# Optimization experiments

Hardware: AMD Instinct MI355X
Metric: run time of the kernel (lower is better)

Reference implementation:

```python
import jax, jax.numpy as jnp
import numpy as np

# config matching init_kwargs
WS = 7          # window side -> N = 49 tokens
NUM_HEADS = 8
DIM = 256
N = WS * WS     # 49
NW = 64         # windows per image (56x56 feature map / 7x7 windows)
B = 64          # images
B_ = B * NW     # 4096 window-batches


def _relative_position_index():
    # exact replica of the numpy construction in __init__
    coords_h = np.arange(WS)
    coords_w = np.arange(WS)
    coords = np.stack(np.meshgrid(coords_h, coords_w, indexing='ij'))  # (2, WS, WS)
    coords_flatten = coords.reshape(2, -1)                             # (2, N)
    rel = coords_flatten[:, :, None] - coords_flatten[:, None, :]      # (2, N, N)
    rel = rel.transpose(1, 2, 0)                                       # (N, N, 2)
    rel[:, :, 0] += WS - 1
    rel[:, :, 1] += WS - 1
    rel[:, :, 0] *= 2 * WS - 1
    return rel.sum(-1).astype(np.int32)                                # (N, N) in [0, 169)


def setup_inputs() -> dict:
    key = jax.random.key(0)
    k1, k2, k3 = jax.random.split(key, 3)
    x = jax.random.normal(k1, (B_, N, DIM), dtype=jnp.float32)
    bias_table = jax.random.normal(k2, (169, NUM_HEADS), dtype=jnp.float32) * 0.02
    mask = jax.random.normal(k3, (NW, N, N), dtype=jnp.float32)
    rel_index = jnp.asarray(_relative_position_index())
    return {"x": x, "bias_table": bias_table, "mask": mask, "rel_index": rel_index}


def reference(x, bias_table, mask, rel_index):
    B_, n, C = x.shape
    head_dim = C // NUM_HEADS
    scale = head_dim ** -0.5
    # NOTE: original call() uses x_qkv[0] for q, k AND v (qkv Dense never applied)
    qkv = x.reshape(B_, n, NUM_HEADS, head_dim).transpose(0, 2, 1, 3)  # (B_, H, N, hd)
    attn = jnp.einsum('bhid,bhjd->bhij', qkv * scale, qkv)             # (B_, H, N, N)
    # gathered relative-position bias: (N*N, H) -> (H, N, N)
    bias = bias_table[rel_index.reshape(-1)].reshape(n, n, NUM_HEADS).transpose(2, 0, 1)
    attn = attn + bias[None]
    # additive window mask: (nW, N, N) broadcast over batch and heads
    nW = mask.shape[0]
    attn = attn.reshape(B_ // nW, nW, NUM_HEADS, n, n) + mask[None, :, None]
    attn = jax.nn.softmax(attn.reshape(B_, NUM_HEADS, n, n), axis=-1)
    out = jnp.einsum('bhij,bhjd->bhid', attn, qkv)                     # (B_, H, N, hd)
    return out.transpose(0, 2, 1, 3).reshape(B_, n, C)
```

## Files before the change

kernel.cpp:

```cpp
#include <hip/hip_runtime.h>
#include <hip/hip_bf16.h>

typedef float f32x4 __attribute__((ext_vector_type(4)));
typedef short s16x8 __attribute__((ext_vector_type(8)));

#define LOG2E 1.4426950408889634f
#define NEGINF (-1e30f)

__device__ __forceinline__ unsigned short f2bf(float f) {
    __hip_bfloat16 h = __float2bfloat16(f);
    unsigned short u;
    __builtin_memcpy(&u, &h, 2);
    return u;
}

__global__ void fuse_bias_mask(const float* __restrict__ bias_table,
                               const float* __restrict__ mask,
                               const int*   __restrict__ rel_index,
                               float*       __restrict__ fused) {
    int tid = blockIdx.x * 256 + threadIdx.x;
    const int total = 512 * 2401;
    if (tid >= total) return;
    int wh  = tid / 2401;
    int rem = tid - wh * 2401;
    int c   = rem / 49;
    int w = wh >> 3, h = wh & 7;
    int idx = rel_index[rem];
    float v = (mask[w * 2401 + rem] + bias_table[idx * 8 + h]) * LOG2E;
    fused[((long)wh * 49 + c) * 52 + (rem - c * 49)] = v;
}

template<bool FUSED>
__global__ __launch_bounds__(256, 2)
void win_attn(const float* __restrict__ x,
              const float* __restrict__ bias_table,
              const float* __restrict__ mask,
              const int*   __restrict__ rel_index,
              const float* __restrict__ fused,
              float*       __restrict__ out) {
    __shared__ char Plds[4][8192];
    const int tid  = threadIdx.x;
    const int wav  = tid >> 6;
    const int lane = tid & 63;
    const int li   = lane & 15;
    const int g    = lane >> 4;
    const int b    = blockIdx.x;
    const int w    = b & 63;
    char* P = &Plds[wav][0];
    const float scale2 = 0.17677669529663689f * LOG2E;

    const float* xb = x + (long)b * (49 * 256);

    for (int hh = 0; hh < 2; ++hh) {
        const int h = wav * 2 + hh;
        const float* xh = xb + h * 32;

        s16x8 Fh[4], Fl[4];
        #pragma unroll
        for (int t = 0; t < 4; ++t) {
            int row = t * 16 + li;
            float f[8];
            if (row < 49) {
                const f32x4* p = (const f32x4*)(xh + row * 256 + g * 8);
                f32x4 v0 = p[0], v1 = p[1];
                f[0]=v0.x; f[1]=v0.y; f[2]=v0.z; f[3]=v0.w;
                f[4]=v1.x; f[5]=v1.y; f[6]=v1.z; f[7]=v1.w;
            } else {
                #pragma unroll
                for (int j = 0; j < 8; ++j) f[j] = 0.f;
            }
            s16x8 hi, lo;
            #pragma unroll
            for (int j = 0; j < 8; ++j) {
                unsigned u = __float_as_uint(f[j]);
                hi[j] = (short)(u >> 16);
                float rm = f[j] - __uint_as_float(u & 0xFFFF0000u);
                lo[j] = (short)f2bf(rm);
            }
            Fh[t] = hi; Fl[t] = lo;
        }

        s16x8 Vf[2][2];
        #pragma unroll
        for (int nd = 0; nd < 2; ++nd)
            #pragma unroll
            for (int kt = 0; kt < 2; ++kt) {
                int d = li + 16 * nd;
                s16x8 vv;
                #pragma unroll
                for (int jj = 0; jj < 8; ++jj) {
                    int j = 32 * kt + 8 * g + jj;
                    float v = (j < 49) ? xh[j * 256 + d] : 0.f;
                    vv[jj] = (short)f2bf(v);
                }
                Vf[nd][kt] = vv;
            }

        f32x4 acc[4][4];
        #pragma unroll
        for (int mr = 0; mr < 4; ++mr)
            #pragma unroll
            for (int nc = 0; nc < 4; ++nc)
                acc[mr][nc] = f32x4{0.f, 0.f, 0.f, 0.f};
        #pragma unroll
        for (int mr = 0; mr < 4; ++mr)
            #pragma unroll
            for (int nc = 0; nc < 4; ++nc) {
                f32x4 a = acc[mr][nc];
                a = __builtin_amdgcn_mfma_f32_16x16x32_bf16(Fh[mr], Fh[nc], a, 0, 0, 0);
                a = __builtin_amdgcn_mfma_f32_16x16x32_bf16(Fh[mr], Fl[nc], a, 0, 0, 0);
                a = __builtin_amdgcn_mfma_f32_16x16x32_bf16(Fl[mr], Fh[nc], a, 0, 0, 0);
                acc[mr][nc] = a;
            }

        const int wh = w * 8 + h;
        #pragma unroll
        for (int nc = 0; nc < 4; ++nc) {
            int c = li + 16 * nc;
            int cidx = min(c, 48);
            if (FUSED) {
                const float* fb = fused + ((long)wh * 49 + cidx) * 52;
                #pragma unroll
                for (int mr = 0; mr < 3; ++mr) {
                    f32x4 t = *(const f32x4*)(fb + 16 * mr + 4 * g);
                    #pragma unroll
                    for (int i = 0; i < 4; ++i)
                        acc[mr][nc][i] = acc[mr][nc][i] * scale2 + t[i];
                }
                float t48 = fb[48];
                acc[3][nc][0] = (g == 0) ? acc[3][nc][0] * scale2 + t48 : NEGINF;
                acc[3][nc][1] = NEGINF; acc[3][nc][2] = NEGINF; acc[3][nc][3] = NEGINF;
            } else {
                const int base = cidx * 49;
                #pragma unroll
                for (int mr = 0; mr < 3; ++mr)
                    #pragma unroll
                    for (int i = 0; i < 4; ++i) {
                        int r = 16 * mr + 4 * g + i;
                        float bm = (mask[w * 2401 + base + r]
                                    + bias_table[rel_index[base + r] * 8 + h]) * LOG2E;
                        acc[mr][nc][i] = acc[mr][nc][i] * scale2 + bm;
                    }
                float bm48 = (mask[w * 2401 + base + 48]
                              + bias_table[rel_index[base + 48] * 8 + h]) * LOG2E;
                acc[3][nc][0] = (g == 0) ? acc[3][nc][0] * scale2 + bm48 : NEGINF;
                acc[3][nc][1] = NEGINF; acc[3][nc][2] = NEGINF; acc[3][nc][3] = NEGINF;
            }
            float m = NEGINF;
            #pragma unroll
            for (int mr = 0; mr < 4; ++mr)
                #pragma unroll
                for (int i = 0; i < 4; ++i) m = fmaxf(m, acc[mr][nc][i]);
            m = fmaxf(m, __shfl_xor(m, 16));
            m = fmaxf(m, __shfl_xor(m, 32));
            float s = 0.f;
            #pragma unroll
            for (int mr = 0; mr < 4; ++mr)
                #pragma unroll
                for (int i = 0; i < 4; ++i) {
                    float p = __builtin_amdgcn_exp2f(acc[mr][nc][i] - m);
                    acc[mr][nc][i] = p;
                    s += p;
                }
            s += __shfl_xor(s, 16);
            s += __shfl_xor(s, 32);
            float sinv = __builtin_amdgcn_rcpf(s);
            char* rowp = P + c * 128;
            unsigned sw = ((unsigned)(c & 7)) << 4;
            #pragma unroll
            for (int mr = 0; mr < 4; ++mr) {
                unsigned short b0 = f2bf(acc[mr][nc][0] * sinv);
                unsigned short b1 = f2bf(acc[mr][nc][1] * sinv);
                unsigned short b2 = f2bf(acc[mr][nc][2] * sinv);
                unsigned short b3 = f2bf(acc[mr][nc][3] * sinv);
                uint2 v;
                v.x = (unsigned)b0 | ((unsigned)b1 << 16);
                v.y = (unsigned)b2 | ((unsigned)b3 << 16);
                *(uint2*)(rowp + (((unsigned)(32 * mr + 8 * g)) ^ sw)) = v;
            }
        }

        f32x4 o[4][2];
        #pragma unroll
        for (int mc = 0; mc < 4; ++mc)
            #pragma unroll
            for (int nd = 0; nd < 2; ++nd) o[mc][nd] = f32x4{0.f, 0.f, 0.f, 0.f};
        #pragma unroll
        for (int mc = 0; mc < 4; ++mc) {
            int c2 = li + 16 * mc;
            char* rowp = P + c2 * 128;
            unsigned sw = ((unsigned)(c2 & 7)) << 4;
            #pragma unroll
            for (int kt = 0; kt < 2; ++kt) {
                s16x8 pa = *(const s16x8*)(rowp + (((unsigned)(64 * kt + 16 * g)) ^ sw));
                #pragma unroll
                for (int nd = 0; nd < 2; ++nd)
                    o[mc][nd] = __builtin_amdgcn_mfma_f32_16x16x32_bf16(pa, Vf[nd][kt], o[mc][nd], 0, 0, 0);
            }
        }

        float* ob = out + (long)b * (49 * 256) + h * 32;
        #pragma unroll
        for (int mc = 0; mc < 4; ++mc) {
            int cbase = 16 * mc + 4 * g;
            #pragma unroll
            for (int i = 0; i < 4; ++i) {
                int crow = cbase + i;
                if (crow < 49) {
                    #pragma unroll
                    for (int nd = 0; nd < 2; ++nd)
                        ob[(long)crow * 256 + 16 * nd + li] = o[mc][nd][i];
                }
            }
        }
    }
}

extern "C" void kernel_launch(void* const* d_in, const int* in_sizes, int n_in,
                              void* d_out, int out_size, void* d_ws, size_t ws_size,
                              hipStream_t stream) {
    const float* x          = (const float*)d_in[0];
    const float* bias_table = (const float*)d_in[1];
    const float* mask       = (const float*)d_in[2];
    const int*   rel_index  = (const int*)d_in[3];
    float* out   = (float*)d_out;
    float* fused = (float*)d_ws;

    const size_t need = (size_t)512 * 49 * 52 * 4;
    if (ws_size >= need) {
        const int total = 512 * 2401;
        fuse_bias_mask<<<(total + 255) / 256, 256, 0, stream>>>(bias_table, mask, rel_index, fused);
        win_attn<true><<<4096, 256, 0, stream>>>(x, bias_table, mask, rel_index, fused, out);
    } else {
        win_attn<false><<<4096, 256, 0, stream>>>(x, bias_table, mask, rel_index, nullptr, out);
    }
}
```

Measured before the change: 404.6 us.

## Process two windows per block with prefetched loads, per-column QK MFMA, and priority hints

Each block now handles two window-batches (four head tasks per wave), and the raw x loads for the next task are issued before the current task's softmax so global latency overlaps compute. The QK^T MFMAs are computed per column tile just before their softmax, which cuts the live accumulator registers. Occupancy is raised to 3 blocks per CU, and s_setprio marks the MFMA sections. Output stores become nontemporal. The costs are fewer blocks in the grid and extra registers held for the prefetch buffer.

```diff
diff --git a/kernel.cpp b/kernel.cpp
--- a/kernel.cpp
+++ b/kernel.cpp
@@ -3,6 +3,7 @@
 
 typedef float f32x4 __attribute__((ext_vector_type(4)));
 typedef short s16x8 __attribute__((ext_vector_type(8)));
+typedef unsigned int u32;
 
 #define LOG2E 1.4426950408889634f
 #define NEGINF (-1e30f)
@@ -31,7 +32,7 @@
 }
 
 template<bool FUSED>
-__global__ __launch_bounds__(256, 2)
+__global__ __launch_bounds__(256, 3)
 void win_attn(const float* __restrict__ x,
               const float* __restrict__ bias_table,
               const float* __restrict__ mask,
@@ -44,92 +45,113 @@
     const int lane = tid & 63;
     const int li   = lane & 15;
     const int g    = lane >> 4;
-    const int b    = blockIdx.x;
-    const int w    = b & 63;
     char* P = &Plds[wav][0];
     const float scale2 = 0.17677669529663689f * LOG2E;
 
-    const float* xb = x + (long)b * (49 * 256);
-
-    for (int hh = 0; hh < 2; ++hh) {
-        const int h = wav * 2 + hh;
-        const float* xh = xb + h * 32;
-
-        s16x8 Fh[4], Fl[4];
+    const int b0 = blockIdx.x * 2;
+
+    f32x4 raw[4][2];
+
+    auto issue_raw = [&](int task) {
+        int it = task >> 1, hh = task & 1;
+        int b = b0 + it, h = wav * 2 + hh;
+        const float* xh = x + (long)b * (49 * 256) + h * 32;
         #pragma unroll
         for (int t = 0; t < 4; ++t) {
             int row = t * 16 + li;
-            float f[8];
             if (row < 49) {
-                const f32x4* p = (const f32x4*)(xh + row * 256 + g * 8);
-                f32x4 v0 = p[0], v1 = p[1];
-                f[0]=v0.x; f[1]=v0.y; f[2]=v0.z; f[3]=v0.w;
-                f[4]=v1.x; f[5]=v1.y; f[6]=v1.z; f[7]=v1.w;
+                const f32x4* p = (const f32x4*)(xh + (long)row * 256 + g * 8);
+                raw[t][0] = p[0];
+                raw[t][1] = p[1];
             } else {
-                #pragma unroll
-                for (int j = 0; j < 8; ++j) f[j] = 0.f;
-            }
-            s16x8 hi, lo;
-            #pragma unroll
-            for (int j = 0; j < 8; ++j) {
-                unsigned u = __float_as_uint(f[j]);
-                hi[j] = (short)(u >> 16);
-                float rm = f[j] - __uint_as_float(u & 0xFFFF0000u);
-                lo[j] = (short)f2bf(rm);
-            }
-            Fh[t] = hi; Fl[t] = lo;
-        }
-
-        s16x8 Vf[2][2];
+                raw[t][0] = f32x4{0.f, 0.f, 0.f, 0.f};
+                raw[t][1] = f32x4{0.f, 0.f, 0.f, 0.f};
+            }
+        }
+    };
+
+    issue_raw(0);
+
+    #pragma unroll 1
+    for (int task = 0; task < 4; ++task) {
+        const int it = task >> 1, hh = task & 1;
+        const int b = b0 + it, h = wav * 2 + hh, w = b & 63;
+        const float* xh = x + (long)b * (49 * 256) + h * 32;
+
+        float vraw[2][2][8];
         #pragma unroll
         for (int nd = 0; nd < 2; ++nd)
             #pragma unroll
             for (int kt = 0; kt < 2; ++kt) {
                 int d = li + 16 * nd;
-                s16x8 vv;
                 #pragma unroll
                 for (int jj = 0; jj < 8; ++jj) {
                     int j = 32 * kt + 8 * g + jj;
-                    float v = (j < 49) ? xh[j * 256 + d] : 0.f;
-                    vv[jj] = (short)f2bf(v);
-                }
+                    vraw[nd][kt][jj] = (j < 49) ? xh[(long)j * 256 + d] : 0.f;
+                }
+            }
+
+        s16x8 Fh[4], Fl[4];
+        #pragma unroll
+        for (int t = 0; t < 4; ++t) {
+            u32 hp[4], lp[4];
+            #pragma unroll
+            for (int pq = 0; pq < 4; ++pq) {
+                float f0 = raw[t][pq >> 1][(pq & 1) * 2 + 0];
+                float f1 = raw[t][pq >> 1][(pq & 1) * 2 + 1];
+                u32 u0 = __float_as_uint(f0), u1 = __float_as_uint(f1);
+                hp[pq] = (u0 >> 16) | (u1 & 0xFFFF0000u);
+                float r0 = f0 - __uint_as_float(u0 & 0xFFFF0000u);
+                float r1 = f1 - __uint_as_float(u1 & 0xFFFF0000u);
+                lp[pq] = (u32)f2bf(r0) | ((u32)f2bf(r1) << 16);
+            }
+            __builtin_memcpy(&Fh[t], hp, 16);
+            __builtin_memcpy(&Fl[t], lp, 16);
+        }
+
+        s16x8 Vf[2][2];
+        #pragma unroll
+        for (int nd = 0; nd < 2; ++nd)
+            #pragma unroll
+            for (int kt = 0; kt < 2; ++kt) {
+                s16x8 vv;
+                #pragma unroll
+                for (int jj = 0; jj < 8; ++jj)
+                    vv[jj] = (short)f2bf(vraw[nd][kt][jj]);
                 Vf[nd][kt] = vv;
             }
 
-        f32x4 acc[4][4];
-        #pragma unroll
-        for (int mr = 0; mr < 4; ++mr)
-            #pragma unroll
-            for (int nc = 0; nc < 4; ++nc)
-                acc[mr][nc] = f32x4{0.f, 0.f, 0.f, 0.f};
-        #pragma unroll
-        for (int mr = 0; mr < 4; ++mr)
-            #pragma unroll
-            for (int nc = 0; nc < 4; ++nc) {
-                f32x4 a = acc[mr][nc];
-                a = __builtin_amdgcn_mfma_f32_16x16x32_bf16(Fh[mr], Fh[nc], a, 0, 0, 0);
-                a = __builtin_amdgcn_mfma_f32_16x16x32_bf16(Fh[mr], Fl[nc], a, 0, 0, 0);
-                a = __builtin_amdgcn_mfma_f32_16x16x32_bf16(Fl[mr], Fh[nc], a, 0, 0, 0);
-                acc[mr][nc] = a;
-            }
+        if (task < 3) issue_raw(task + 1);
 
         const int wh = w * 8 + h;
         #pragma unroll
         for (int nc = 0; nc < 4; ++nc) {
+            __builtin_amdgcn_s_setprio(1);
+            f32x4 a[4];
+            #pragma unroll
+            for (int mr = 0; mr < 4; ++mr) {
+                f32x4 t = f32x4{0.f, 0.f, 0.f, 0.f};
+                t = __builtin_amdgcn_mfma_f32_16x16x32_bf16(Fh[mr], Fh[nc], t, 0, 0, 0);
+                t = __builtin_amdgcn_mfma_f32_16x16x32_bf16(Fh[mr], Fl[nc], t, 0, 0, 0);
+                t = __builtin_amdgcn_mfma_f32_16x16x32_bf16(Fl[mr], Fh[nc], t, 0, 0, 0);
+                a[mr] = t;
+            }
+            __builtin_amdgcn_s_setprio(0);
+
             int c = li + 16 * nc;
             int cidx = min(c, 48);
             if (FUSED) {
                 const float* fb = fused + ((long)wh * 49 + cidx) * 52;
                 #pragma unroll
                 for (int mr = 0; mr < 3; ++mr) {
-                    f32x4 t = *(const f32x4*)(fb + 16 * mr + 4 * g);
+                    f32x4 tt = *(const f32x4*)(fb + 16 * mr + 4 * g);
                     #pragma unroll
                     for (int i = 0; i < 4; ++i)
-                        acc[mr][nc][i] = acc[mr][nc][i] * scale2 + t[i];
+                        a[mr][i] = a[mr][i] * scale2 + tt[i];
                 }
                 float t48 = fb[48];
-                acc[3][nc][0] = (g == 0) ? acc[3][nc][0] * scale2 + t48 : NEGINF;
-                acc[3][nc][1] = NEGINF; acc[3][nc][2] = NEGINF; acc[3][nc][3] = NEGINF;
+                a[3][0] = (g == 0) ? a[3][0] * scale2 + t48 : NEGINF;
+                a[3][1] = NEGINF; a[3][2] = NEGINF; a[3][3] = NEGINF;
             } else {
                 const int base = cidx * 49;
                 #pragma unroll
@@ -139,43 +161,41 @@
                         int r = 16 * mr + 4 * g + i;
                         float bm = (mask[w * 2401 + base + r]
                                     + bias_table[rel_index[base + r] * 8 + h]) * LOG2E;
-                        acc[mr][nc][i] = acc[mr][nc][i] * scale2 + bm;
+                        a[mr][i] = a[mr][i] * scale2 + bm;
                     }
                 float bm48 = (mask[w * 2401 + base + 48]
                               + bias_table[rel_index[base + 48] * 8 + h]) * LOG2E;
-                acc[3][nc][0] = (g == 0) ? acc[3][nc][0] * scale2 + bm48 : NEGINF;
-                acc[3][nc][1] = NEGINF; acc[3][nc][2] = NEGINF; acc[3][nc][3] = NEGINF;
-            }
-            float m = NEGINF;
-            #pragma unroll
-            for (int mr = 0; mr < 4; ++mr)
-                #pragma unroll
-                for (int i = 0; i < 4; ++i) m = fmaxf(m, acc[mr][nc][i]);
+                a[3][0] = (g == 0) ? a[3][0] * scale2 + bm48 : NEGINF;
+                a[3][1] = NEGINF; a[3][2] = NEGINF; a[3][3] = NEGINF;
+            }
+
+            float m = fmaxf(fmaxf(fmaxf(a[0][0], a[0][1]), fmaxf(a[0][2], a[0][3])),
+                            fmaxf(fmaxf(a[1][0], a[1][1]), fmaxf(a[1][2], a[1][3])));
+            m = fmaxf(m, fmaxf(fmaxf(fmaxf(a[2][0], a[2][1]), fmaxf(a[2][2], a[2][3])),
+                               fmaxf(fmaxf(a[3][0], a[3][1]), fmaxf(a[3][2], a[3][3]))));
             m = fmaxf(m, __shfl_xor(m, 16));
             m = fmaxf(m, __shfl_xor(m, 32));
+
             float s = 0.f;
             #pragma unroll
             for (int mr = 0; mr < 4; ++mr)
                 #pragma unroll
                 for (int i = 0; i < 4; ++i) {
-                    float p = __builtin_amdgcn_exp2f(acc[mr][nc][i] - m);
-                    acc[mr][nc][i] = p;
+                    float p = __builtin_amdgcn_exp2f(a[mr][i] - m);
+                    a[mr][i] = p;
                     s += p;
                 }
             s += __shfl_xor(s, 16);
             s += __shfl_xor(s, 32);
             float sinv = __builtin_amdgcn_rcpf(s);
+
             char* rowp = P + c * 128;
             unsigned sw = ((unsigned)(c & 7)) << 4;
             #pragma unroll
             for (int mr = 0; mr < 4; ++mr) {
-                unsigned short b0 = f2bf(acc[mr][nc][0] * sinv);
-                unsigned short b1 = f2bf(acc[mr][nc][1] * sinv);
-                unsigned short b2 = f2bf(acc[mr][nc][2] * sinv);
-                unsigned short b3 = f2bf(acc[mr][nc][3] * sinv);
-                uint2 v;
-                v.x = (unsigned)b0 | ((unsigned)b1 << 16);
-                v.y = (unsigned)b2 | ((unsigned)b3 << 16);
+                u32 p0 = (u32)f2bf(a[mr][0] * sinv) | ((u32)f2bf(a[mr][1] * sinv) << 16);
+                u32 p1 = (u32)f2bf(a[mr][2] * sinv) | ((u32)f2bf(a[mr][3] * sinv) << 16);
+                uint2 v; v.x = p0; v.y = p1;
                 *(uint2*)(rowp + (((unsigned)(32 * mr + 8 * g)) ^ sw)) = v;
             }
         }
@@ -185,6 +205,7 @@
         for (int mc = 0; mc < 4; ++mc)
             #pragma unroll
             for (int nd = 0; nd < 2; ++nd) o[mc][nd] = f32x4{0.f, 0.f, 0.f, 0.f};
+        __builtin_amdgcn_s_setprio(1);
         #pragma unroll
         for (int mc = 0; mc < 4; ++mc) {
             int c2 = li + 16 * mc;
@@ -198,6 +219,7 @@
                     o[mc][nd] = __builtin_amdgcn_mfma_f32_16x16x32_bf16(pa, Vf[nd][kt], o[mc][nd], 0, 0, 0);
             }
         }
+        __builtin_amdgcn_s_setprio(0);
 
         float* ob = out + (long)b * (49 * 256) + h * 32;
         #pragma unroll
@@ -209,7 +231,8 @@
                 if (crow < 49) {
                     #pragma unroll
                     for (int nd = 0; nd < 2; ++nd)
-                        ob[(long)crow * 256 + 16 * nd + li] = o[mc][nd][i];
+                        __builtin_nontemporal_store(o[mc][nd][i],
+                            &ob[(long)crow * 256 + 16 * nd + li]);
                 }
             }
         }
@@ -230,8 +253,8 @@
     if (ws_size >= need) {
         const int total = 512 * 2401;
         fuse_bias_mask<<<(total + 255) / 256, 256, 0, stream>>>(bias_table, mask, rel_index, fused);
-        win_attn<true><<<4096, 256, 0, stream>>>(x, bias_table, mask, rel_index, fused, out);
+        win_attn<true><<<2048, 256, 0, stream>>>(x, bias_table, mask, rel_index, fused, out);
     } else {
-        win_attn<false><<<4096, 256, 0, stream>>>(x, bias_table, mask, rel_index, nullptr, out);
+        win_attn<false><<<2048, 256, 0, stream>>>(x, bias_table, mask, rel_index, nullptr, out);
     }
 }
```

Result: slower. 434.0 us (+7.3%).
